# Performance work log

Measured on AMD Instinct MI355X. Metric: run time of the kernel, lower is better.

Reference implementation:

```python
import jax, jax.numpy as jnp
import numpy as np

WDIM = 16
NBATCH = 1024
N = 4096
DF = 2 * WDIM  # Wishart degrees of freedom


def setup_inputs() -> dict:
    key = jax.random.key(0)
    k1, k2, k3 = jax.random.split(key, 3)
    # strict-lower-triangular noise for the Bartlett factor
    A_noise = jax.random.normal(k1, (NBATCH, WDIM, WDIM), dtype=jnp.float32)
    # Chi2(df - i) draws for the diagonal: chi2(k) = 2 * Gamma(k/2)
    a = (DF - jnp.arange(WDIM, dtype=jnp.float32)) / 2.0  # [wdim]
    chisq = (2.0 * jax.random.gamma(k2, a, (NBATCH, WDIM))).astype(jnp.float32)
    # final standard-normal draw applied to the normalized inverse factor
    z = jax.random.normal(k3, (NBATCH, N, WDIM), dtype=jnp.float32)
    return {"A_noise": A_noise, "chisq": chisq, "z": z}


def reference(A_noise, chisq, z):
    # Bartlett cholesky factor of Wishart(I, 2*wdim): lower-tri with sqrt(chi2) diag.
    # (V = I so L = chol(V) = I and the original L @ A is a no-op.)
    eye = jnp.eye(WDIM, dtype=A_noise.dtype)
    A = jnp.tril(A_noise, -1) + jnp.sqrt(chisq)[:, :, None] * eye  # [b, p, p]
    # A = inverse(sample).transpose(-2, -1)
    At = jnp.swapaxes(jnp.linalg.inv(A), -1, -2)  # [b, p, p]
    # diag(At @ At^T)^(-1/2) = rsqrt of row norms squared
    scale = jax.lax.rsqrt(jnp.sum(At * At, axis=-1))  # [b, p]
    M = scale[:, :, None] * At  # diag_embed(scale) @ At, [b, p, p]
    # w = (M broadcast over n) @ z[..., None], squeezed -> [b, n, p]
    w = jnp.einsum('bij,bnj->bni', M, z)
    return w
```

## Files before the change

kernel.cpp:

```cpp
#include <hip/hip_runtime.h>

#define NB 1024
#define NN 4096
#define P  16
#define TPB 256
#define RPT 8
#define SEGB (NN * 4)
#define BPB  (SEGB / (TPB * RPT))

typedef float f4 __attribute__((ext_vector_type(4)));

__global__ __launch_bounds__(TPB) void prior_w_fused(
    const float* __restrict__ A_noise, const float* __restrict__ chisq,
    const float* __restrict__ z, float* __restrict__ w) {
  __shared__ __align__(16) float Msh[P][P];
  __shared__ float As[P][P + 1];
  __shared__ float colS[P][P + 1];
  __shared__ float dS[P];

  const int tid   = threadIdx.x;
  const int b     = blockIdx.x >> 3;
  const int chunk = blockIdx.x & 7;
  const int q     = tid & 3;
  const int quad0 = tid & ~3;

  const size_t segbase = (size_t)b * SEGB + (size_t)chunk * (TPB * RPT) + tid;
  const f4* zf4 = (const f4*)z;
  f4 zv[RPT];
#pragma unroll
  for (int k = 0; k < RPT; ++k)
    zv[k] = __builtin_nontemporal_load(zf4 + segbase + (size_t)k * TPB);

  As[tid >> 4][tid & 15] = A_noise[(size_t)b * (P * P) + tid];
  if (tid < P) dS[tid] = rsqrtf(chisq[(size_t)b * P + tid]);
  __syncthreads();

  if (tid < P) {
    const int j = tid;
    const float cj = dS[j];
    colS[j][j] = cj;
    float n2 = cj * cj;
    for (int i = j + 1; i < P; ++i) {
      float s = 0.f;
      for (int k = j; k < i; ++k) s += As[i][k] * colS[j][k];
      const float ci = -s * dS[i];
      colS[j][i] = ci;
      n2 += ci * ci;
    }
    const float sc = rsqrtf(n2);
    for (int i = 0; i < j; ++i) Msh[j][i] = 0.f;
    for (int i = j; i < P; ++i) Msh[j][i] = sc * colS[j][i];
  }
  __syncthreads();

  f4 Mr[4][4];
#pragma unroll
  for (int c = 0; c < 4; ++c)
#pragma unroll
    for (int s = 0; s < 4; ++s)
      Mr[c][s] = *(const f4*)&Msh[4 * q + c][4 * s];

  f4* wf4 = (f4*)w;
#pragma unroll
  for (int k = 0; k < RPT; ++k) {
    f4 row[4];
#pragma unroll
    for (int d = 0; d < 4; ++d) {
      row[d].x = __shfl(zv[k].x, quad0 + d, 64);
      row[d].y = __shfl(zv[k].y, quad0 + d, 64);
      row[d].z = __shfl(zv[k].z, quad0 + d, 64);
      row[d].w = __shfl(zv[k].w, quad0 + d, 64);
    }
    f4 o;
#pragma unroll
    for (int c = 0; c < 4; ++c) {
      float acc = 0.f;
#pragma unroll
      for (int s = 0; s < 4; ++s) {
        acc = fmaf(Mr[c][s].x, row[s].x, acc);
        acc = fmaf(Mr[c][s].y, row[s].y, acc);
        acc = fmaf(Mr[c][s].z, row[s].z, acc);
        acc = fmaf(Mr[c][s].w, row[s].w, acc);
      }
      if (c == 0) o.x = acc; else if (c == 1) o.y = acc;
      else if (c == 2) o.z = acc; else o.w = acc;
    }
    __builtin_nontemporal_store(o, wf4 + segbase + (size_t)k * TPB);
  }
}

extern "C" void kernel_launch(void* const* d_in, const int* in_sizes, int n_in,
                              void* d_out, int out_size, void* d_ws, size_t ws_size,
                              hipStream_t stream) {
  const float* A_noise = (const float*)d_in[0];
  const float* chisq   = (const float*)d_in[1];
  const float* z       = (const float*)d_in[2];
  prior_w_fused<<<NB * BPB, TPB, 0, stream>>>(A_noise, chisq, z, (float*)d_out);
}
```

Measured before the change: 441.9 us.

## Use one block per batch with double-buffered z loads across chunks

The grid changes from eight blocks per batch to one block per batch, and each block now loops over sixteen chunks. Loads of the next chunk of z go into a second register buffer while the current chunk is computed and stored. This avoids recomputing the 16x16 triangular inverse in eight blocks per batch and overlaps memory latency with compute. In exchange the grid shrinks to 1024 blocks, which cuts memory-level parallelism and leaves the per-block setup exposed, and launch bounds now ask for four blocks per CU.

```diff
diff --git a/kernel.cpp b/kernel.cpp
--- a/kernel.cpp
+++ b/kernel.cpp
@@ -4,13 +4,13 @@
 #define NN 4096
 #define P  16
 #define TPB 256
-#define RPT 8
+#define RPT 4
+#define NCHUNK 16
 #define SEGB (NN * 4)
-#define BPB  (SEGB / (TPB * RPT))
 
 typedef float f4 __attribute__((ext_vector_type(4)));
 
-__global__ __launch_bounds__(TPB) void prior_w_fused(
+__global__ __launch_bounds__(TPB, 4) void prior_w_fused(
     const float* __restrict__ A_noise, const float* __restrict__ chisq,
     const float* __restrict__ z, float* __restrict__ w) {
   __shared__ __align__(16) float Msh[P][P];
@@ -19,17 +19,18 @@
   __shared__ float dS[P];
 
   const int tid   = threadIdx.x;
-  const int b     = blockIdx.x >> 3;
-  const int chunk = blockIdx.x & 7;
+  const int b     = blockIdx.x;
   const int q     = tid & 3;
   const int quad0 = tid & ~3;
 
-  const size_t segbase = (size_t)b * SEGB + (size_t)chunk * (TPB * RPT) + tid;
+  const size_t base = (size_t)b * SEGB + tid;
   const f4* zf4 = (const f4*)z;
-  f4 zv[RPT];
+  f4* wf4 = (f4*)w;
+
+  f4 zA[RPT], zB[RPT];
 #pragma unroll
   for (int k = 0; k < RPT; ++k)
-    zv[k] = __builtin_nontemporal_load(zf4 + segbase + (size_t)k * TPB);
+    zA[k] = __builtin_nontemporal_load(zf4 + base + (size_t)k * TPB);
 
   As[tid >> 4][tid & 15] = A_noise[(size_t)b * (P * P) + tid];
   if (tid < P) dS[tid] = rsqrtf(chisq[(size_t)b * P + tid]);
@@ -60,32 +61,52 @@
     for (int s = 0; s < 4; ++s)
       Mr[c][s] = *(const f4*)&Msh[4 * q + c][4 * s];
 
-  f4* wf4 = (f4*)w;
+  auto do_chunk = [&](const f4 (&zv)[RPT], int c) {
+    const size_t sb = base + (size_t)c * (TPB * RPT);
 #pragma unroll
-  for (int k = 0; k < RPT; ++k) {
-    f4 row[4];
+    for (int k = 0; k < RPT; ++k) {
+      f4 row[4];
 #pragma unroll
-    for (int d = 0; d < 4; ++d) {
-      row[d].x = __shfl(zv[k].x, quad0 + d, 64);
-      row[d].y = __shfl(zv[k].y, quad0 + d, 64);
-      row[d].z = __shfl(zv[k].z, quad0 + d, 64);
-      row[d].w = __shfl(zv[k].w, quad0 + d, 64);
+      for (int d = 0; d < 4; ++d) {
+        row[d].x = __shfl(zv[k].x, quad0 + d, 64);
+        row[d].y = __shfl(zv[k].y, quad0 + d, 64);
+        row[d].z = __shfl(zv[k].z, quad0 + d, 64);
+        row[d].w = __shfl(zv[k].w, quad0 + d, 64);
+      }
+      f4 o;
+#pragma unroll
+      for (int cc = 0; cc < 4; ++cc) {
+        float acc = 0.f;
+#pragma unroll
+        for (int s = 0; s < 4; ++s) {
+          acc = fmaf(Mr[cc][s].x, row[s].x, acc);
+          acc = fmaf(Mr[cc][s].y, row[s].y, acc);
+          acc = fmaf(Mr[cc][s].z, row[s].z, acc);
+          acc = fmaf(Mr[cc][s].w, row[s].w, acc);
+        }
+        if (cc == 0) o.x = acc; else if (cc == 1) o.y = acc;
+        else if (cc == 2) o.z = acc; else o.w = acc;
+      }
+      __builtin_nontemporal_store(o, wf4 + sb + (size_t)k * TPB);
     }
-    f4 o;
+  };
+
+#pragma unroll 1
+  for (int c = 0; c < NCHUNK; c += 2) {
+    if (c + 1 < NCHUNK) {
+      const size_t sb = base + (size_t)(c + 1) * (TPB * RPT);
 #pragma unroll
-    for (int c = 0; c < 4; ++c) {
-      float acc = 0.f;
+      for (int k = 0; k < RPT; ++k)
+        zB[k] = __builtin_nontemporal_load(zf4 + sb + (size_t)k * TPB);
+    }
+    do_chunk(zA, c);
+    if (c + 2 < NCHUNK) {
+      const size_t sb = base + (size_t)(c + 2) * (TPB * RPT);
 #pragma unroll
-      for (int s = 0; s < 4; ++s) {
-        acc = fmaf(Mr[c][s].x, row[s].x, acc);
-        acc = fmaf(Mr[c][s].y, row[s].y, acc);
-        acc = fmaf(Mr[c][s].z, row[s].z, acc);
-        acc = fmaf(Mr[c][s].w, row[s].w, acc);
-      }
-      if (c == 0) o.x = acc; else if (c == 1) o.y = acc;
-      else if (c == 2) o.z = acc; else o.w = acc;
+      for (int k = 0; k < RPT; ++k)
+        zA[k] = __builtin_nontemporal_load(zf4 + sb + (size_t)k * TPB);
     }
-    __builtin_nontemporal_store(o, wf4 + segbase + (size_t)k * TPB);
+    do_chunk(zB, c + 1);
   }
 }
 
@@ -95,5 +116,5 @@
   const float* A_noise = (const float*)d_in[0];
   const float* chisq   = (const float*)d_in[1];
   const float* z       = (const float*)d_in[2];
-  prior_w_fused<<<NB * BPB, TPB, 0, stream>>>(A_noise, chisq, z, (float*)d_out);
+  prior_w_fused<<<NB, TPB, 0, stream>>>(A_noise, chisq, z, (float*)d_out);
 }
```

Measured after the change: 448.0 us. About the same (+1.4%).
